# Performance work log

Hardware: AMD Instinct MI355X
Metric: run time of the kernel (lower is better)

Reference implementation:

```python
import jax, jax.numpy as jnp
import numpy as np

B = 262144
INPUT_SIZE = 128
HIDDEN_SIZE = 128
EPS = 1e-08


def rms_norm(x, eps=EPS):
    # NB: despite the name, the original subtracts the mean (LayerNorm without affine)
    mean = jnp.mean(x, axis=-1, keepdims=True)
    var = jnp.var(x, axis=-1, keepdims=True)  # biased, matches unbiased=False
    return (x - mean) / jnp.sqrt(var + eps)


def activation_quant(x):
    s = 127.0 / jnp.max(jnp.abs(x), axis=-1, keepdims=True)
    return jnp.clip(jnp.round(s * x), -128.0, 127.0) / s


def matmul_free_linear(x, w_t):
    # w_t is ternary {-1,0,1}, shape [in, out]; original uses two masked matmuls
    pos = (w_t == 1.0).astype(x.dtype)
    neg = (w_t == -1.0).astype(x.dtype)
    return x @ pos - x @ neg


def setup_inputs() -> dict:
    key = jax.random.key(0)
    k1, k2, k3, k4, k5 = jax.random.split(key, 5)
    return {
        "x_t": jax.random.normal(k1, (B, INPUT_SIZE), dtype=jnp.float32),
        "h_t_minus_1": jax.random.normal(k2, (B, HIDDEN_SIZE), dtype=jnp.float32),
        "W_f": jax.random.normal(k3, (HIDDEN_SIZE, INPUT_SIZE), dtype=jnp.float32) * 0.01,
        "W_c": jax.random.normal(k4, (HIDDEN_SIZE, INPUT_SIZE), dtype=jnp.float32) * 0.01,
        "W_g": jax.random.normal(k5, (HIDDEN_SIZE, INPUT_SIZE), dtype=jnp.float32) * 0.01,
        "b_f": jnp.zeros((HIDDEN_SIZE,), dtype=jnp.float32),
        "b_c": jnp.zeros((HIDDEN_SIZE,), dtype=jnp.float32),
        "b_g": jnp.zeros((HIDDEN_SIZE,), dtype=jnp.float32),
    }


def reference(x_t, h_t_minus_1, W_f, W_c, W_g, b_f, b_c, b_g):
    x = activation_quant(rms_norm(x_t, EPS))
    Wf_t = jnp.sign(W_f).T  # [in, hidden]
    Wc_t = jnp.sign(W_c).T
    Wg_t = jnp.sign(W_g).T
    f_t = jax.nn.sigmoid(matmul_free_linear(x, Wf_t) + b_f)
    c_t = jax.nn.silu(matmul_free_linear(x, Wc_t) + b_c)
    g_t = jax.nn.sigmoid(matmul_free_linear(x, Wg_t) + b_g)
    h_t = f_t * h_t_minus_1 + (1.0 - f_t) * c_t
    o_t = g_t * h_t
    return (o_t, h_t)
```

## Files before the change

### kernel.cpp

```cpp
#include <hip/hip_runtime.h>
#include <math.h>

typedef __attribute__((ext_vector_type(4))) int   i32x4;
typedef __attribute__((ext_vector_type(4))) float f32x4;

__device__ __forceinline__ float sigmoidf_(float v) {
    return 1.0f / (1.0f + __expf(-v));
}

__global__ __launch_bounds__(256, 3)
void mlgru_kernel(const float* __restrict__ x,
                  const float* __restrict__ hprev,
                  const float* __restrict__ Wf,
                  const float* __restrict__ Wc,
                  const float* __restrict__ Wg,
                  const float* __restrict__ bf,
                  const float* __restrict__ bc,
                  const float* __restrict__ bg,
                  float* __restrict__ out,
                  int nrows)
{
    __shared__ i32x4 wlds[3 * 8 * 2 * 64];

    const int tid  = threadIdx.x;
    const int lane = tid & 63;
    const int widx = tid >> 6;
    const int lm   = lane & 15;
    const int kg   = lane >> 4;

    for (int idx = tid; idx < 3 * 8 * 2 * 64; idx += 256) {
        const int l  = idx & 63;
        const int s  = (idx >> 6) & 1;
        const int t  = (idx >> 7) & 7;
        const int g  = idx >> 10;
        const float* Wp = (g == 0) ? Wf : ((g == 1) ? Wc : Wg);
        const int n  = t * 16 + (l & 15);
        const int kb = s * 64 + (l >> 4) * 16;
        i32x4 fr;
        #pragma unroll
        for (int d = 0; d < 4; ++d) {
            const float4 v = *(const float4*)(Wp + n * 128 + kb + d * 4);
            const int b0 = (v.x > 0.f) - (v.x < 0.f);
            const int b1 = (v.y > 0.f) - (v.y < 0.f);
            const int b2 = (v.z > 0.f) - (v.z < 0.f);
            const int b3 = (v.w > 0.f) - (v.w < 0.f);
            fr[d] = (b0 & 0xFF) | ((b1 & 0xFF) << 8) | ((b2 & 0xFF) << 16) | ((b3 & 0xFF) << 24);
        }
        wlds[idx] = fr;
    }

    float vbf[8], vbc[8], vbg[8];
    #pragma unroll
    for (int t = 0; t < 8; ++t) {
        vbf[t] = bf[t * 16 + lm];
        vbc[t] = bc[t * 16 + lm];
        vbg[t] = bg[t * 16 + lm];
    }
    __syncthreads();

    const int gw   = blockIdx.x * 4 + widx;
    const int nw   = gridDim.x * 4;
    const int ngrp = nrows >> 5;
    const long long hoff = (long long)nrows * 128;

    for (int grp = gw; grp < ngrp; grp += nw) {
        const int row0 = grp << 5;

        i32x4 afrag[2][2];
        float invm[2];

        #pragma unroll
        for (int mt = 0; mt < 2; ++mt) {
            const float* xr = x + (long long)(row0 + mt * 16 + lm) * 128 + kg * 16;
            f32x4 vv[8];
            #pragma unroll
            for (int j = 0; j < 4; ++j) {
                vv[j]     = *(const f32x4*)(xr + j * 4);
                vv[j + 4] = *(const f32x4*)(xr + 64 + j * 4);
            }
            float s = 0.f, ss = 0.f;
            #pragma unroll
            for (int j = 0; j < 8; ++j)
                #pragma unroll
                for (int e = 0; e < 4; ++e) { const float t = vv[j][e]; s += t; ss = fmaf(t, t, ss); }
            s  += __shfl_xor(s, 16);   ss += __shfl_xor(ss, 16);
            s  += __shfl_xor(s, 32);   ss += __shfl_xor(ss, 32);
            const float mean = s * (1.0f / 128.0f);
            const float var  = ss * (1.0f / 128.0f) - mean * mean;
            const float rstd = rsqrtf(var + 1e-8f);
            float am = 0.f;
            #pragma unroll
            for (int j = 0; j < 8; ++j)
                #pragma unroll
                for (int e = 0; e < 4; ++e) {
                    const float t = vv[j][e] - mean;
                    vv[j][e] = t;
                    am = fmaxf(am, fabsf(t));
                }
            am = fmaxf(am, __shfl_xor(am, 16));
            am = fmaxf(am, __shfl_xor(am, 32));
            const float sq = 127.0f / am;
            invm[mt] = am * rstd * (1.0f / 127.0f);
            #pragma unroll
            for (int s2 = 0; s2 < 2; ++s2) {
                i32x4 fr;
                #pragma unroll
                for (int d = 0; d < 4; ++d) {
                    const int j = s2 * 4 + d;
                    const int q0 = max(-128, min(127, (int)rintf(vv[j][0] * sq)));
                    const int q1 = max(-128, min(127, (int)rintf(vv[j][1] * sq)));
                    const int q2 = max(-128, min(127, (int)rintf(vv[j][2] * sq)));
                    const int q3 = max(-128, min(127, (int)rintf(vv[j][3] * sq)));
                    fr[d] = (q0 & 0xFF) | ((q1 & 0xFF) << 8) | ((q2 & 0xFF) << 16) | ((q3 & 0xFF) << 24);
                }
                afrag[mt][s2] = fr;
            }
        }

        float invb[2][4];
        #pragma unroll
        for (int mt = 0; mt < 2; ++mt)
            #pragma unroll
            for (int r = 0; r < 4; ++r)
                invb[mt][r] = __shfl(invm[mt], kg * 4 + r);

        for (int t = 0; t < 8; ++t) {
            i32x4 acc[3][2];
            #pragma unroll
            for (int g = 0; g < 3; ++g) {
                acc[g][0] = (i32x4){0, 0, 0, 0};
                acc[g][1] = (i32x4){0, 0, 0, 0};
            }
            #pragma unroll
            for (int s2 = 0; s2 < 2; ++s2)
                #pragma unroll
                for (int g = 0; g < 3; ++g) {
                    const i32x4 bfr = wlds[((g * 8 + t) * 2 + s2) * 64 + lane];
                    acc[g][0] = __builtin_amdgcn_mfma_i32_16x16x64_i8(afrag[0][s2], bfr, acc[g][0], 0, 0, 0);
                    acc[g][1] = __builtin_amdgcn_mfma_i32_16x16x64_i8(afrag[1][s2], bfr, acc[g][1], 0, 0, 0);
                }

            #pragma unroll
            for (int mt = 0; mt < 2; ++mt)
                #pragma unroll
                for (int r = 0; r < 4; ++r) {
                    const int m = kg * 4 + r;
                    const float inv = invb[mt][r];
                    const long long rbase =
                        (long long)(row0 + mt * 16 + m) * 128 + t * 16 + lm;
                    const float hp = hprev[rbase];
                    const float fx = (float)acc[0][mt][r] * inv + vbf[t];
                    const float cx = (float)acc[1][mt][r] * inv + vbc[t];
                    const float gx = (float)acc[2][mt][r] * inv + vbg[t];
                    const float f  = sigmoidf_(fx);
                    const float c  = cx * sigmoidf_(cx);
                    const float gg = sigmoidf_(gx);
                    const float h  = f * hp + (1.0f - f) * c;
                    out[rbase]        = gg * h;
                    out[hoff + rbase] = h;
                }
        }
    }
}

extern "C" void kernel_launch(void* const* d_in, const int* in_sizes, int n_in,
                              void* d_out, int out_size, void* d_ws, size_t ws_size,
                              hipStream_t stream) {
    const float* x  = (const float*)d_in[0];
    const float* h  = (const float*)d_in[1];
    const float* Wf = (const float*)d_in[2];
    const float* Wc = (const float*)d_in[3];
    const float* Wg = (const float*)d_in[4];
    const float* bf = (const float*)d_in[5];
    const float* bc = (const float*)d_in[6];
    const float* bg = (const float*)d_in[7];
    float* out = (float*)d_out;
    const int nrows = in_sizes[0] / 128;

    hipLaunchKernelGGL(mlgru_kernel, dim3(1024), dim3(256), 0, stream,
                       x, h, Wf, Wc, Wg, bf, bc, bg, out, nrows);
}
```

Measured before the change: 515.0 us.

## Launch one 32-row group per wave and prefetch hprev/bias one tile ahead

Replaces the persistent grid-stride loop with a grid sized so that each wave handles exactly one 32-row group, using 512-thread blocks. The hidden-tile loop is fully unrolled, and the next tile's hprev values and biases (now kept in LDS) are software-prefetched while the current tile's MFMAs and epilogue run. The int8 clamp is dropped, and indexing moves from 64-bit to 32-bit. In exchange, every block repeats the weight sign-packing into LDS, which adds redundant setup work across many more blocks, and register pressure rises.

```diff
diff --git a/kernel.cpp b/kernel.cpp
--- a/kernel.cpp
+++ b/kernel.cpp
@@ -8,7 +8,7 @@
     return 1.0f / (1.0f + __expf(-v));
 }
 
-__global__ __launch_bounds__(256, 3)
+__global__ __launch_bounds__(512, 6)
 void mlgru_kernel(const float* __restrict__ x,
                   const float* __restrict__ hprev,
                   const float* __restrict__ Wf,
@@ -21,6 +21,7 @@
                   int nrows)
 {
     __shared__ i32x4 wlds[3 * 8 * 2 * 64];
+    __shared__ float blds[3 * 128];
 
     const int tid  = threadIdx.x;
     const int lane = tid & 63;
@@ -28,7 +29,7 @@
     const int lm   = lane & 15;
     const int kg   = lane >> 4;
 
-    for (int idx = tid; idx < 3 * 8 * 2 * 64; idx += 256) {
+    for (int idx = tid; idx < 3 * 8 * 2 * 64; idx += 512) {
         const int l  = idx & 63;
         const int s  = (idx >> 6) & 1;
         const int t  = (idx >> 7) & 7;
@@ -48,118 +49,136 @@
         }
         wlds[idx] = fr;
     }
-
-    float vbf[8], vbc[8], vbg[8];
+    if (tid < 384)
+        blds[tid] = (tid < 128) ? bf[tid] : (tid < 256) ? bc[tid - 128] : bg[tid - 256];
+    __syncthreads();
+
+    const int ngrp = nrows >> 5;
+    const int grp  = blockIdx.x * 8 + widx;
+    if (grp >= ngrp) return;
+    const int row0 = grp << 5;
+    const int hoff = nrows * 128;
+
+    i32x4 afrag[2][2];
+    float invm[2];
+
+    #pragma unroll
+    for (int mt = 0; mt < 2; ++mt) {
+        const float* xr = x + (row0 + mt * 16 + lm) * 128 + kg * 16;
+        f32x4 vv[8];
+        #pragma unroll
+        for (int j = 0; j < 4; ++j) {
+            vv[j]     = *(const f32x4*)(xr + j * 4);
+            vv[j + 4] = *(const f32x4*)(xr + 64 + j * 4);
+        }
+        float s = 0.f, ss = 0.f;
+        #pragma unroll
+        for (int j = 0; j < 8; ++j)
+            #pragma unroll
+            for (int e = 0; e < 4; ++e) { const float t = vv[j][e]; s += t; ss = fmaf(t, t, ss); }
+        s  += __shfl_xor(s, 16);   ss += __shfl_xor(ss, 16);
+        s  += __shfl_xor(s, 32);   ss += __shfl_xor(ss, 32);
+        const float mean = s * (1.0f / 128.0f);
+        const float var  = ss * (1.0f / 128.0f) - mean * mean;
+        const float rstd = rsqrtf(var + 1e-8f);
+        float am = 0.f;
+        #pragma unroll
+        for (int j = 0; j < 8; ++j)
+            #pragma unroll
+            for (int e = 0; e < 4; ++e) {
+                const float t = vv[j][e] - mean;
+                vv[j][e] = t;
+                am = fmaxf(am, fabsf(t));
+            }
+        am = fmaxf(am, __shfl_xor(am, 16));
+        am = fmaxf(am, __shfl_xor(am, 32));
+        const float sq = 127.0f / am;
+        invm[mt] = am * rstd * (1.0f / 127.0f);
+        #pragma unroll
+        for (int s2 = 0; s2 < 2; ++s2) {
+            i32x4 fr;
+            #pragma unroll
+            for (int d = 0; d < 4; ++d) {
+                const int j = s2 * 4 + d;
+                const int q0 = (int)rintf(vv[j][0] * sq);
+                const int q1 = (int)rintf(vv[j][1] * sq);
+                const int q2 = (int)rintf(vv[j][2] * sq);
+                const int q3 = (int)rintf(vv[j][3] * sq);
+                fr[d] = (q0 & 0xFF) | ((q1 & 0xFF) << 8) | ((q2 & 0xFF) << 16) | ((q3 & 0xFF) << 24);
+            }
+            afrag[mt][s2] = fr;
+        }
+    }
+
+    float invb[2][4];
+    #pragma unroll
+    for (int mt = 0; mt < 2; ++mt)
+        #pragma unroll
+        for (int r = 0; r < 4; ++r)
+            invb[mt][r] = __shfl(invm[mt], kg * 4 + r);
+
+    const int cb0 = (row0 + kg * 4) * 128 + lm;
+    float hp[2][4];
+    #pragma unroll
+    for (int mt = 0; mt < 2; ++mt)
+        #pragma unroll
+        for (int r = 0; r < 4; ++r)
+            hp[mt][r] = hprev[cb0 + mt * 2048 + r * 128];
+    float bft = blds[lm], bct = blds[128 + lm], bgt = blds[256 + lm];
+
     #pragma unroll
     for (int t = 0; t < 8; ++t) {
-        vbf[t] = bf[t * 16 + lm];
-        vbc[t] = bc[t * 16 + lm];
-        vbg[t] = bg[t * 16 + lm];
-    }
-    __syncthreads();
-
-    const int gw   = blockIdx.x * 4 + widx;
-    const int nw   = gridDim.x * 4;
-    const int ngrp = nrows >> 5;
-    const long long hoff = (long long)nrows * 128;
-
-    for (int grp = gw; grp < ngrp; grp += nw) {
-        const int row0 = grp << 5;
-
-        i32x4 afrag[2][2];
-        float invm[2];
-
-        #pragma unroll
-        for (int mt = 0; mt < 2; ++mt) {
-            const float* xr = x + (long long)(row0 + mt * 16 + lm) * 128 + kg * 16;
-            f32x4 vv[8];
-            #pragma unroll
-            for (int j = 0; j < 4; ++j) {
-                vv[j]     = *(const f32x4*)(xr + j * 4);
-                vv[j + 4] = *(const f32x4*)(xr + 64 + j * 4);
-            }
-            float s = 0.f, ss = 0.f;
-            #pragma unroll
-            for (int j = 0; j < 8; ++j)
-                #pragma unroll
-                for (int e = 0; e < 4; ++e) { const float t = vv[j][e]; s += t; ss = fmaf(t, t, ss); }
-            s  += __shfl_xor(s, 16);   ss += __shfl_xor(ss, 16);
-            s  += __shfl_xor(s, 32);   ss += __shfl_xor(ss, 32);
-            const float mean = s * (1.0f / 128.0f);
-            const float var  = ss * (1.0f / 128.0f) - mean * mean;
-            const float rstd = rsqrtf(var + 1e-8f);
-            float am = 0.f;
-            #pragma unroll
-            for (int j = 0; j < 8; ++j)
-                #pragma unroll
-                for (int e = 0; e < 4; ++e) {
-                    const float t = vv[j][e] - mean;
-                    vv[j][e] = t;
-                    am = fmaxf(am, fabsf(t));
-                }
-            am = fmaxf(am, __shfl_xor(am, 16));
-            am = fmaxf(am, __shfl_xor(am, 32));
-            const float sq = 127.0f / am;
-            invm[mt] = am * rstd * (1.0f / 127.0f);
-            #pragma unroll
-            for (int s2 = 0; s2 < 2; ++s2) {
-                i32x4 fr;
-                #pragma unroll
-                for (int d = 0; d < 4; ++d) {
-                    const int j = s2 * 4 + d;
-                    const int q0 = max(-128, min(127, (int)rintf(vv[j][0] * sq)));
-                    const int q1 = max(-128, min(127, (int)rintf(vv[j][1] * sq)));
-                    const int q2 = max(-128, min(127, (int)rintf(vv[j][2] * sq)));
-                    const int q3 = max(-128, min(127, (int)rintf(vv[j][3] * sq)));
-                    fr[d] = (q0 & 0xFF) | ((q1 & 0xFF) << 8) | ((q2 & 0xFF) << 16) | ((q3 & 0xFF) << 24);
-                }
-                afrag[mt][s2] = fr;
-            }
-        }
-
-        float invb[2][4];
-        #pragma unroll
-        for (int mt = 0; mt < 2; ++mt)
-            #pragma unroll
-            for (int r = 0; r < 4; ++r)
-                invb[mt][r] = __shfl(invm[mt], kg * 4 + r);
-
-        for (int t = 0; t < 8; ++t) {
-            i32x4 acc[3][2];
+        i32x4 acc[3][2];
+        #pragma unroll
+        for (int g = 0; g < 3; ++g) {
+            acc[g][0] = (i32x4){0, 0, 0, 0};
+            acc[g][1] = (i32x4){0, 0, 0, 0};
+        }
+        #pragma unroll
+        for (int s2 = 0; s2 < 2; ++s2)
             #pragma unroll
             for (int g = 0; g < 3; ++g) {
-                acc[g][0] = (i32x4){0, 0, 0, 0};
-                acc[g][1] = (i32x4){0, 0, 0, 0};
-            }
-            #pragma unroll
-            for (int s2 = 0; s2 < 2; ++s2)
-                #pragma unroll
-                for (int g = 0; g < 3; ++g) {
-                    const i32x4 bfr = wlds[((g * 8 + t) * 2 + s2) * 64 + lane];
-                    acc[g][0] = __builtin_amdgcn_mfma_i32_16x16x64_i8(afrag[0][s2], bfr, acc[g][0], 0, 0, 0);
-                    acc[g][1] = __builtin_amdgcn_mfma_i32_16x16x64_i8(afrag[1][s2], bfr, acc[g][1], 0, 0, 0);
-                }
-
+                const i32x4 bfr = wlds[((g * 8 + t) * 2 + s2) * 64 + lane];
+                acc[g][0] = __builtin_amdgcn_mfma_i32_16x16x64_i8(afrag[0][s2], bfr, acc[g][0], 0, 0, 0);
+                acc[g][1] = __builtin_amdgcn_mfma_i32_16x16x64_i8(afrag[1][s2], bfr, acc[g][1], 0, 0, 0);
+            }
+
+        float hpn[2][4], bfn = 0.f, bcn = 0.f, bgn = 0.f;
+        if (t < 7) {
+            const int nb = cb0 + (t + 1) * 16;
             #pragma unroll
             for (int mt = 0; mt < 2; ++mt)
                 #pragma unroll
-                for (int r = 0; r < 4; ++r) {
-                    const int m = kg * 4 + r;
-                    const float inv = invb[mt][r];
-                    const long long rbase =
-                        (long long)(row0 + mt * 16 + m) * 128 + t * 16 + lm;
-                    const float hp = hprev[rbase];
-                    const float fx = (float)acc[0][mt][r] * inv + vbf[t];
-                    const float cx = (float)acc[1][mt][r] * inv + vbc[t];
-                    const float gx = (float)acc[2][mt][r] * inv + vbg[t];
-                    const float f  = sigmoidf_(fx);
-                    const float c  = cx * sigmoidf_(cx);
-                    const float gg = sigmoidf_(gx);
-                    const float h  = f * hp + (1.0f - f) * c;
-                    out[rbase]        = gg * h;
-                    out[hoff + rbase] = h;
-                }
-        }
+                for (int r = 0; r < 4; ++r)
+                    hpn[mt][r] = hprev[nb + mt * 2048 + r * 128];
+            bfn = blds[(t + 1) * 16 + lm];
+            bcn = blds[128 + (t + 1) * 16 + lm];
+            bgn = blds[256 + (t + 1) * 16 + lm];
+        }
+
+        #pragma unroll
+        for (int mt = 0; mt < 2; ++mt)
+            #pragma unroll
+            for (int r = 0; r < 4; ++r) {
+                const float inv = invb[mt][r];
+                const int rbase = cb0 + mt * 2048 + r * 128 + t * 16;
+                const float fx = (float)acc[0][mt][r] * inv + bft;
+                const float cx = (float)acc[1][mt][r] * inv + bct;
+                const float gx = (float)acc[2][mt][r] * inv + bgt;
+                const float f  = sigmoidf_(fx);
+                const float c  = cx * sigmoidf_(cx);
+                const float gg = sigmoidf_(gx);
+                const float h  = f * hp[mt][r] + (1.0f - f) * c;
+                out[rbase]        = gg * h;
+                out[hoff + rbase] = h;
+            }
+
+        #pragma unroll
+        for (int mt = 0; mt < 2; ++mt)
+            #pragma unroll
+            for (int r = 0; r < 4; ++r)
+                hp[mt][r] = hpn[mt][r];
+        bft = bfn; bct = bcn; bgt = bgn;
     }
 }
 
@@ -176,7 +195,9 @@
     const float* bg = (const float*)d_in[7];
     float* out = (float*)d_out;
     const int nrows = in_sizes[0] / 128;
-
-    hipLaunchKernelGGL(mlgru_kernel, dim3(1024), dim3(256), 0, stream,
+    const int ngrp  = nrows >> 5;
+    const int nblk  = (ngrp + 7) / 8;
+
+    hipLaunchKernelGGL(mlgru_kernel, dim3(nblk), dim3(512), 0, stream,
                        x, h, Wf, Wc, Wg, bf, bc, bg, out, nrows);
 }
```

Measured after the change: 598.4 us. 1.16x slower.
